# Kernel tuning notes

Hardware: AMD Instinct MI355X
Metric: run time of the kernel (lower is better)

Reference implementation:

```python
import jax, jax.numpy as jnp
import numpy as np

B, N_CLASS, N_CENTER, HIDDEN = 1024, 50, 8, 512
INIT_MU, BETA, EPS = 0.1, 0.5, 1e-8


def setup_inputs() -> dict:
    key = jax.random.key(0)
    k1, k2, k3, k4 = jax.random.split(key, 4)
    x = jax.random.normal(k1, (B, HIDDEN), dtype=jnp.float32)
    # class_mu ~ U(-init_mu, init_mu), matching torch.rand(...) * 2*init_mu - init_mu
    class_mu = jax.random.uniform(k2, (N_CLASS, N_CENTER, HIDDEN),
                                  minval=-INIT_MU, maxval=INIT_MU, dtype=jnp.float32)
    # binary dropout-style mask: (rand > beta).float()
    mask = (jax.random.uniform(k3, (N_CENTER, HIDDEN)) > BETA).astype(jnp.float32)
    # fixed random projection W ~ 0.1 * N(0,1)
    W = jax.random.normal(k4, (HIDDEN, HIDDEN), dtype=jnp.float32) * 0.1
    return {"x": x, "class_mu": class_mu, "mask": mask, "W": W}


def reference(x, class_mu, mask, W):
    # [B, n_center, hidden]: per-center masked copy of x, then shared projection W
    masked = x[:, None, :] * mask[None, :, :]
    mul = jnp.einsum('bch,hd->bcd', masked, W)
    # broadcast squared-distance against cluster centers: [B, n_class, n_center]
    diff = mul[:, None, :, :] - class_mu[None, :, :, :]  # [B, K, C, H]
    score = 1.0 / (1.0 + jnp.sum(diff * diff, axis=-1))  # Student-t style kernel
    # normalize over n_center (dim 2)
    distances = score / (jnp.sum(score, axis=2, keepdims=True) + EPS)
    # k_assign: second normalization over last dim (n_center)
    k_assign = distances / jnp.sum(distances, axis=-1, keepdims=True)
    return (mul, k_assign, distances)
```

## Files before the change

### kernel.cpp

```cpp
#include <hip/hip_runtime.h>

typedef short s16x8 __attribute__((ext_vector_type(8)));
typedef float f32x4 __attribute__((ext_vector_type(4)));

#define NB      1024
#define NCLASS  50
#define NCENTER 8
#define HID     512
#define KPAD    64
#define MROWS   8192

#define OFF_ABF    0u
#define OFF_WT     8388608u
#define OFF_MUBF   8912896u
#define OFF_MUNORM 9437184u
#define OFF_MULBF  9439232u
#define OFF_SCORE  17827840u

#define OUT_KA 4194304
#define OUT_D  4603904

__device__ __forceinline__ short f2bf(float f) {
    unsigned int u = __float_as_uint(f);
    unsigned int r = (u + 0x7FFFu + ((u >> 16) & 1u)) >> 16;
    return (short)(unsigned short)r;
}
__device__ __forceinline__ float bf2f(short h) {
    return __uint_as_float(((unsigned int)(unsigned short)h) << 16);
}

__global__ __launch_bounds__(256) void prep_kernel(
    const float* __restrict__ x, const float* __restrict__ class_mu,
    const float* __restrict__ mask, const float* __restrict__ W,
    short* __restrict__ Abf, short* __restrict__ WT,
    short* __restrict__ Mubf, float* __restrict__ Munorm)
{
    __shared__ float lds[64][65];
    const int blk = blockIdx.x, tid = threadIdx.x;

    if (blk < 256) {
        #pragma unroll
        for (int i = 0; i < 8; ++i) {
            int g = (blk * 256 + tid) + i * 65536;
            int e = g * 8;
            int r = e >> 9;
            int k = e & 511;
            int b = r >> 3, c = r & 7;
            const float4* xp = (const float4*)(x + b * HID + k);
            const float4* mp = (const float4*)(mask + c * HID + k);
            float4 x0 = xp[0], x1 = xp[1];
            float4 m0 = mp[0], m1 = mp[1];
            s16x8 o;
            o[0] = f2bf(x0.x * m0.x); o[1] = f2bf(x0.y * m0.y);
            o[2] = f2bf(x0.z * m0.z); o[3] = f2bf(x0.w * m0.w);
            o[4] = f2bf(x1.x * m1.x); o[5] = f2bf(x1.y * m1.y);
            o[6] = f2bf(x1.z * m1.z); o[7] = f2bf(x1.w * m1.w);
            *(s16x8*)(Abf + e) = o;
        }
    } else if (blk < 320) {
        int t = blk - 256;
        int th = t & 7, td = t >> 3;
        int col = tid & 63, rb = tid >> 6;
        #pragma unroll
        for (int it = 0; it < 16; ++it) {
            int row = it * 4 + rb;
            lds[row][col] = W[(th * 64 + row) * HID + td * 64 + col];
        }
        __syncthreads();
        #pragma unroll
        for (int it = 0; it < 16; ++it) {
            int row = it * 4 + rb;
            WT[(td * 64 + row) * HID + th * 64 + col] = f2bf(lds[col][row]);
        }
    } else {
        int w = (blk - 320) * 4 + (tid >> 6);
        int lane = tid & 63;
        int c = w >> 6, kk = w & 63;
        int h = lane * 8;
        float v[8];
        if (kk < NCLASS) {
            const float4* p = (const float4*)(class_mu + (kk * NCENTER + c) * HID + h);
            float4 a = p[0], bq = p[1];
            v[0] = a.x;  v[1] = a.y;  v[2] = a.z;  v[3] = a.w;
            v[4] = bq.x; v[5] = bq.y; v[6] = bq.z; v[7] = bq.w;
        } else {
            #pragma unroll
            for (int j = 0; j < 8; ++j) v[j] = 0.f;
        }
        s16x8 o; float sq = 0.f;
        #pragma unroll
        for (int j = 0; j < 8; ++j) { o[j] = f2bf(v[j]); sq += v[j] * v[j]; }
        *(s16x8*)(Mubf + (c * KPAD + kk) * HID + h) = o;
        sq += __shfl_xor(sq, 1);  sq += __shfl_xor(sq, 2);  sq += __shfl_xor(sq, 4);
        sq += __shfl_xor(sq, 8);  sq += __shfl_xor(sq, 16); sq += __shfl_xor(sq, 32);
        if (lane == 0) Munorm[c * KPAD + kk] = sq;
    }
}

__global__ __launch_bounds__(256) void gemm_mul(
    const short* __restrict__ Abf, const short* __restrict__ WT,
    float* __restrict__ mul_out, short* __restrict__ mulbf)
{
    __shared__ short As[128 * 32];
    __shared__ short Bs[128 * 32];
    const int tid = threadIdx.x;
    const int bm = blockIdx.x * 128;
    const int bn = blockIdx.y * 128;
    const int wave = tid >> 6, lane = tid & 63;
    const int wm = (wave & 1) * 64, wn = (wave >> 1) * 64;
    const int q = lane >> 4, l16 = lane & 15;

    f32x4 acc[4][4] = {};

    const int r0 = tid >> 2, c0 = (tid & 3) * 8;

    for (int it = 0; it < 16; ++it) {
        const int k0 = it * 32;
        *(s16x8*)(As + r0 * 32 + c0)        = *(const s16x8*)(Abf + (bm + r0) * HID + k0 + c0);
        *(s16x8*)(As + (r0 + 64) * 32 + c0) = *(const s16x8*)(Abf + (bm + r0 + 64) * HID + k0 + c0);
        *(s16x8*)(Bs + r0 * 32 + c0)        = *(const s16x8*)(WT + (bn + r0) * HID + k0 + c0);
        *(s16x8*)(Bs + (r0 + 64) * 32 + c0) = *(const s16x8*)(WT + (bn + r0 + 64) * HID + k0 + c0);
        __syncthreads();

        s16x8 af[4], bfr[4];
        #pragma unroll
        for (int mt = 0; mt < 4; ++mt)
            af[mt] = *(const s16x8*)(As + (wm + mt * 16 + l16) * 32 + q * 8);
        #pragma unroll
        for (int nt = 0; nt < 4; ++nt)
            bfr[nt] = *(const s16x8*)(Bs + (wn + nt * 16 + l16) * 32 + q * 8);
        #pragma unroll
        for (int mt = 0; mt < 4; ++mt)
            #pragma unroll
            for (int nt = 0; nt < 4; ++nt)
                acc[mt][nt] = __builtin_amdgcn_mfma_f32_16x16x32_bf16(af[mt], bfr[nt], acc[mt][nt], 0, 0, 0);
        __syncthreads();
    }

    #pragma unroll
    for (int mt = 0; mt < 4; ++mt) {
        #pragma unroll
        for (int nt = 0; nt < 4; ++nt) {
            #pragma unroll
            for (int reg = 0; reg < 4; ++reg) {
                int gr = bm + wm + mt * 16 + q * 4 + reg;
                int gc = bn + wn + nt * 16 + l16;
                float v = acc[mt][nt][reg];
                mul_out[gr * HID + gc] = v;
                mulbf[gr * HID + gc] = f2bf(v);
            }
        }
    }
}

__global__ __launch_bounds__(128) void score_kernel(
    const short* __restrict__ mulbf, const short* __restrict__ Mubf,
    const float* __restrict__ Munorm, float* __restrict__ score)
{
    const int tid = threadIdx.x;
    const int c = blockIdx.x & 7, bt = blockIdx.x >> 3;
    const int wave = tid >> 6, lane = tid & 63;
    const int q = lane >> 4, l16 = lane & 15;
    const int b0 = bt * 32 + wave * 16;

    f32x4 acc[4] = {};
    float nrm = 0.f;

    const short* arow = mulbf + ((b0 + l16) * NCENTER + c) * HID + q * 8;
    const short* brow = Mubf + (c * KPAD + l16) * HID + q * 8;

    for (int it = 0; it < 16; ++it) {
        const int k0 = it * 32;
        s16x8 av  = *(const s16x8*)(arow + k0);
        s16x8 bv0 = *(const s16x8*)(brow + k0);
        s16x8 bv1 = *(const s16x8*)(brow + 16 * HID + k0);
        s16x8 bv2 = *(const s16x8*)(brow + 32 * HID + k0);
        s16x8 bv3 = *(const s16x8*)(brow + 48 * HID + k0);
        #pragma unroll
        for (int j = 0; j < 8; ++j) { float f = bf2f(av[j]); nrm += f * f; }
        acc[0] = __builtin_amdgcn_mfma_f32_16x16x32_bf16(av, bv0, acc[0], 0, 0, 0);
        acc[1] = __builtin_amdgcn_mfma_f32_16x16x32_bf16(av, bv1, acc[1], 0, 0, 0);
        acc[2] = __builtin_amdgcn_mfma_f32_16x16x32_bf16(av, bv2, acc[2], 0, 0, 0);
        acc[3] = __builtin_amdgcn_mfma_f32_16x16x32_bf16(av, bv3, acc[3], 0, 0, 0);
    }

    nrm += __shfl_xor(nrm, 16);
    nrm += __shfl_xor(nrm, 32);
    float rowNorm[4];
    #pragma unroll
    for (int reg = 0; reg < 4; ++reg) rowNorm[reg] = __shfl(nrm, q * 4 + reg);

    #pragma unroll
    for (int nt = 0; nt < 4; ++nt) {
        float mn = Munorm[c * KPAD + nt * 16 + l16];
        #pragma unroll
        for (int reg = 0; reg < 4; ++reg) {
            float sq = rowNorm[reg] + mn - 2.f * acc[nt][reg];
            float sc = 1.f / (1.f + sq);
            int b = b0 + q * 4 + reg;
            int kcls = nt * 16 + l16;
            score[(b * KPAD + kcls) * NCENTER + c] = sc;
        }
    }
}

__global__ __launch_bounds__(256) void norm_kernel(
    const float* __restrict__ score, float* __restrict__ out)
{
    int t = blockIdx.x * 256 + threadIdx.x;
    if (t >= NB * NCLASS) return;
    int b = t / NCLASS, k = t % NCLASS;
    const float4* sp = (const float4*)(score + (b * KPAD + k) * NCENTER);
    float4 s0 = sp[0], s1 = sp[1];
    float S = s0.x + s0.y + s0.z + s0.w + s1.x + s1.y + s1.z + s1.w;
    float invd = 1.f / (S + 1e-8f);
    float invk = 1.f / S;
    float4 ka0, ka1, dd0, dd1;
    ka0.x = s0.x * invk; ka0.y = s0.y * invk; ka0.z = s0.z * invk; ka0.w = s0.w * invk;
    ka1.x = s1.x * invk; ka1.y = s1.y * invk; ka1.z = s1.z * invk; ka1.w = s1.w * invk;
    dd0.x = s0.x * invd; dd0.y = s0.y * invd; dd0.z = s0.z * invd; dd0.w = s0.w * invd;
    dd1.x = s1.x * invd; dd1.y = s1.y * invd; dd1.z = s1.z * invd; dd1.w = s1.w * invd;
    float* kap = out + OUT_KA + (b * NCLASS + k) * NCENTER;
    float* dp  = out + OUT_D  + (b * NCLASS + k) * NCENTER;
    ((float4*)kap)[0] = ka0; ((float4*)kap)[1] = ka1;
    ((float4*)dp)[0]  = dd0; ((float4*)dp)[1]  = dd1;
}

extern "C" void kernel_launch(void* const* d_in, const int* in_sizes, int n_in,
                              void* d_out, int out_size, void* d_ws, size_t ws_size,
                              hipStream_t stream) {
    const float* x        = (const float*)d_in[0];
    const float* class_mu = (const float*)d_in[1];
    const float* mask     = (const float*)d_in[2];
    const float* W        = (const float*)d_in[3];
    float* out = (float*)d_out;
    char* ws = (char*)d_ws;

    short* Abf    = (short*)(ws + OFF_ABF);
    short* WT     = (short*)(ws + OFF_WT);
    short* Mubf   = (short*)(ws + OFF_MUBF);
    float* Munorm = (float*)(ws + OFF_MUNORM);
    short* mulbf  = (short*)(ws + OFF_MULBF);
    float* score  = (float*)(ws + OFF_SCORE);

    prep_kernel<<<448, 256, 0, stream>>>(x, class_mu, mask, W, Abf, WT, Mubf, Munorm);
    gemm_mul<<<dim3(64, 4), 256, 0, stream>>>(Abf, WT, out, mulbf);
    score_kernel<<<256, 128, 0, stream>>>(mulbf, Mubf, Munorm, score);
    norm_kernel<<<200, 256, 0, stream>>>(score, out);
}
```

Before: 97.94 us.

## Fuse mask into GEMM load, compute row norms in epilogue, merge score and normalize

Prep now converts only x to bf16 plus a 16-bit mask, and the GEMM applies the mask with a bitwise AND while loading tiles. This avoids writing and reading the 8x-expanded masked input. The GEMM epilogue computes squared row norms of mul and accumulates them with atomics. The score and normalization kernels are merged into one, which handles all 8 centers per block and writes k_assign and distances directly, removing the intermediate score buffer. The cost is atomic contention, a row norm taken from fp32 accumulators rather than the bf16 values, and a score kernel with only 64 threads per block.

```diff
diff --git a/kernel.cpp b/kernel.cpp
--- a/kernel.cpp
+++ b/kernel.cpp
@@ -2,20 +2,21 @@
 
 typedef short s16x8 __attribute__((ext_vector_type(8)));
 typedef float f32x4 __attribute__((ext_vector_type(4)));
+typedef unsigned int u32x4 __attribute__((ext_vector_type(4)));
 
 #define NB      1024
 #define NCLASS  50
 #define NCENTER 8
 #define HID     512
 #define KPAD    64
-#define MROWS   8192
-
-#define OFF_ABF    0u
-#define OFF_WT     8388608u
-#define OFF_MUBF   8912896u
-#define OFF_MUNORM 9437184u
-#define OFF_MULBF  9439232u
-#define OFF_SCORE  17827840u
+
+#define OFF_XBF    0u
+#define OFF_MASK16 1048576u
+#define OFF_WT     1056768u
+#define OFF_MUBF   1581056u
+#define OFF_MUNT   2105344u
+#define OFF_MULBF  2107392u
+#define OFF_RNORM  10496000u
 
 #define OUT_KA 4194304
 #define OUT_D  4603904
@@ -25,40 +26,50 @@
     unsigned int r = (u + 0x7FFFu + ((u >> 16) & 1u)) >> 16;
     return (short)(unsigned short)r;
 }
-__device__ __forceinline__ float bf2f(short h) {
-    return __uint_as_float(((unsigned int)(unsigned short)h) << 16);
-}
 
 __global__ __launch_bounds__(256) void prep_kernel(
     const float* __restrict__ x, const float* __restrict__ class_mu,
     const float* __restrict__ mask, const float* __restrict__ W,
-    short* __restrict__ Abf, short* __restrict__ WT,
-    short* __restrict__ Mubf, float* __restrict__ Munorm)
+    short* __restrict__ xbf, short* __restrict__ mask16, short* __restrict__ WT,
+    short* __restrict__ Mubf, float* __restrict__ MunormT,
+    float* __restrict__ rowNorm)
 {
     __shared__ float lds[64][65];
     const int blk = blockIdx.x, tid = threadIdx.x;
 
-    if (blk < 256) {
+    if (blk < 32) {
         #pragma unroll
         for (int i = 0; i < 8; ++i) {
-            int g = (blk * 256 + tid) + i * 65536;
+            int g = (blk * 256 + tid) + i * 8192;
             int e = g * 8;
-            int r = e >> 9;
-            int k = e & 511;
-            int b = r >> 3, c = r & 7;
-            const float4* xp = (const float4*)(x + b * HID + k);
-            const float4* mp = (const float4*)(mask + c * HID + k);
-            float4 x0 = xp[0], x1 = xp[1];
-            float4 m0 = mp[0], m1 = mp[1];
+            const float4* xp = (const float4*)(x + e);
+            float4 a = xp[0], b = xp[1];
             s16x8 o;
-            o[0] = f2bf(x0.x * m0.x); o[1] = f2bf(x0.y * m0.y);
-            o[2] = f2bf(x0.z * m0.z); o[3] = f2bf(x0.w * m0.w);
-            o[4] = f2bf(x1.x * m1.x); o[5] = f2bf(x1.y * m1.y);
-            o[6] = f2bf(x1.z * m1.z); o[7] = f2bf(x1.w * m1.w);
-            *(s16x8*)(Abf + e) = o;
-        }
-    } else if (blk < 320) {
-        int t = blk - 256;
+            o[0] = f2bf(a.x); o[1] = f2bf(a.y); o[2] = f2bf(a.z); o[3] = f2bf(a.w);
+            o[4] = f2bf(b.x); o[5] = f2bf(b.y); o[6] = f2bf(b.z); o[7] = f2bf(b.w);
+            *(s16x8*)(xbf + e) = o;
+        }
+    } else if (blk == 32) {
+        int e = tid * 16;
+        const float4* mp = (const float4*)(mask + e);
+        float4 m0 = mp[0], m1 = mp[1], m2 = mp[2], m3 = mp[3];
+        s16x8 o0, o1;
+        o0[0] = (m0.x != 0.f) ? (short)0xFFFF : 0; o0[1] = (m0.y != 0.f) ? (short)0xFFFF : 0;
+        o0[2] = (m0.z != 0.f) ? (short)0xFFFF : 0; o0[3] = (m0.w != 0.f) ? (short)0xFFFF : 0;
+        o0[4] = (m1.x != 0.f) ? (short)0xFFFF : 0; o0[5] = (m1.y != 0.f) ? (short)0xFFFF : 0;
+        o0[6] = (m1.z != 0.f) ? (short)0xFFFF : 0; o0[7] = (m1.w != 0.f) ? (short)0xFFFF : 0;
+        o1[0] = (m2.x != 0.f) ? (short)0xFFFF : 0; o1[1] = (m2.y != 0.f) ? (short)0xFFFF : 0;
+        o1[2] = (m2.z != 0.f) ? (short)0xFFFF : 0; o1[3] = (m2.w != 0.f) ? (short)0xFFFF : 0;
+        o1[4] = (m3.x != 0.f) ? (short)0xFFFF : 0; o1[5] = (m3.y != 0.f) ? (short)0xFFFF : 0;
+        o1[6] = (m3.z != 0.f) ? (short)0xFFFF : 0; o1[7] = (m3.w != 0.f) ? (short)0xFFFF : 0;
+        *(s16x8*)(mask16 + e) = o0;
+        *(s16x8*)(mask16 + e + 8) = o1;
+        float4 z = {0.f, 0.f, 0.f, 0.f};
+        #pragma unroll
+        for (int j = 0; j < 8; ++j)
+            *(float4*)(rowNorm + (j * 256 + tid) * 4) = z;
+    } else if (blk < 97) {
+        int t = blk - 33;
         int th = t & 7, td = t >> 3;
         int col = tid & 63, rb = tid >> 6;
         #pragma unroll
@@ -73,7 +84,7 @@
             WT[(td * 64 + row) * HID + th * 64 + col] = f2bf(lds[col][row]);
         }
     } else {
-        int w = (blk - 320) * 4 + (tid >> 6);
+        int w = (blk - 97) * 4 + (tid >> 6);
         int lane = tid & 63;
         int c = w >> 6, kk = w & 63;
         int h = lane * 8;
@@ -93,13 +104,15 @@
         *(s16x8*)(Mubf + (c * KPAD + kk) * HID + h) = o;
         sq += __shfl_xor(sq, 1);  sq += __shfl_xor(sq, 2);  sq += __shfl_xor(sq, 4);
         sq += __shfl_xor(sq, 8);  sq += __shfl_xor(sq, 16); sq += __shfl_xor(sq, 32);
-        if (lane == 0) Munorm[c * KPAD + kk] = sq;
+        if (lane == 0) MunormT[kk * 8 + c] = sq;
     }
 }
 
 __global__ __launch_bounds__(256) void gemm_mul(
-    const short* __restrict__ Abf, const short* __restrict__ WT,
-    float* __restrict__ mul_out, short* __restrict__ mulbf)
+    const short* __restrict__ xbf, const short* __restrict__ mask16,
+    const short* __restrict__ WT,
+    float* __restrict__ mul_out, short* __restrict__ mulbf,
+    float* __restrict__ rowNorm)
 {
     __shared__ short As[128 * 32];
     __shared__ short Bs[128 * 32];
@@ -113,11 +126,17 @@
     f32x4 acc[4][4] = {};
 
     const int r0 = tid >> 2, c0 = (tid & 3) * 8;
+    const int bA0 = (bm >> 3) + (r0 >> 3);
+    const int bA1 = (bm >> 3) + ((r0 + 64) >> 3);
+    const int cA  = r0 & 7;
 
     for (int it = 0; it < 16; ++it) {
         const int k0 = it * 32;
-        *(s16x8*)(As + r0 * 32 + c0)        = *(const s16x8*)(Abf + (bm + r0) * HID + k0 + c0);
-        *(s16x8*)(As + (r0 + 64) * 32 + c0) = *(const s16x8*)(Abf + (bm + r0 + 64) * HID + k0 + c0);
+        u32x4 ma = *(const u32x4*)(mask16 + cA * HID + k0 + c0);
+        u32x4 x0 = *(const u32x4*)(xbf + bA0 * HID + k0 + c0);
+        u32x4 x1 = *(const u32x4*)(xbf + bA1 * HID + k0 + c0);
+        *(u32x4*)(As + r0 * 32 + c0)        = x0 & ma;
+        *(u32x4*)(As + (r0 + 64) * 32 + c0) = x1 & ma;
         *(s16x8*)(Bs + r0 * 32 + c0)        = *(const s16x8*)(WT + (bn + r0) * HID + k0 + c0);
         *(s16x8*)(Bs + (r0 + 64) * 32 + c0) = *(const s16x8*)(WT + (bn + r0 + 64) * HID + k0 + c0);
         __syncthreads();
@@ -151,79 +170,82 @@
             }
         }
     }
-}
-
-__global__ __launch_bounds__(128) void score_kernel(
+    #pragma unroll
+    for (int mt = 0; mt < 4; ++mt) {
+        #pragma unroll
+        for (int reg = 0; reg < 4; ++reg) {
+            float s = acc[mt][0][reg] * acc[mt][0][reg];
+            s += acc[mt][1][reg] * acc[mt][1][reg];
+            s += acc[mt][2][reg] * acc[mt][2][reg];
+            s += acc[mt][3][reg] * acc[mt][3][reg];
+            s += __shfl_xor(s, 1); s += __shfl_xor(s, 2);
+            s += __shfl_xor(s, 4); s += __shfl_xor(s, 8);
+            if (l16 == 0)
+                atomicAdd(&rowNorm[bm + wm + mt * 16 + q * 4 + reg], s);
+        }
+    }
+}
+
+__global__ __launch_bounds__(64) void scorenorm_kernel(
     const short* __restrict__ mulbf, const short* __restrict__ Mubf,
-    const float* __restrict__ Munorm, float* __restrict__ score)
+    const float* __restrict__ MunormT, const float* __restrict__ rowNorm,
+    float* __restrict__ out)
 {
-    const int tid = threadIdx.x;
-    const int c = blockIdx.x & 7, bt = blockIdx.x >> 3;
-    const int wave = tid >> 6, lane = tid & 63;
+    const int bt = blockIdx.x & 63, cg = blockIdx.x >> 6;
+    const int lane = threadIdx.x & 63;
     const int q = lane >> 4, l16 = lane & 15;
-    const int b0 = bt * 32 + wave * 16;
-
-    f32x4 acc[4] = {};
-    float nrm = 0.f;
-
-    const short* arow = mulbf + ((b0 + l16) * NCENTER + c) * HID + q * 8;
-    const short* brow = Mubf + (c * KPAD + l16) * HID + q * 8;
+    const int b0 = bt * 16, cls0 = cg * 16;
+
+    f32x4 acc[8] = {};
+    const short* arow = mulbf + (b0 + l16) * NCENTER * HID + q * 8;
+    const short* brow = Mubf + (cls0 + l16) * HID + q * 8;
 
     for (int it = 0; it < 16; ++it) {
         const int k0 = it * 32;
-        s16x8 av  = *(const s16x8*)(arow + k0);
-        s16x8 bv0 = *(const s16x8*)(brow + k0);
-        s16x8 bv1 = *(const s16x8*)(brow + 16 * HID + k0);
-        s16x8 bv2 = *(const s16x8*)(brow + 32 * HID + k0);
-        s16x8 bv3 = *(const s16x8*)(brow + 48 * HID + k0);
-        #pragma unroll
-        for (int j = 0; j < 8; ++j) { float f = bf2f(av[j]); nrm += f * f; }
-        acc[0] = __builtin_amdgcn_mfma_f32_16x16x32_bf16(av, bv0, acc[0], 0, 0, 0);
-        acc[1] = __builtin_amdgcn_mfma_f32_16x16x32_bf16(av, bv1, acc[1], 0, 0, 0);
-        acc[2] = __builtin_amdgcn_mfma_f32_16x16x32_bf16(av, bv2, acc[2], 0, 0, 0);
-        acc[3] = __builtin_amdgcn_mfma_f32_16x16x32_bf16(av, bv3, acc[3], 0, 0, 0);
-    }
-
-    nrm += __shfl_xor(nrm, 16);
-    nrm += __shfl_xor(nrm, 32);
-    float rowNorm[4];
+        s16x8 av[8], bv[8];
+        #pragma unroll
+        for (int c = 0; c < 8; ++c) av[c] = *(const s16x8*)(arow + c * HID + k0);
+        #pragma unroll
+        for (int c = 0; c < 8; ++c) bv[c] = *(const s16x8*)(brow + c * KPAD * HID + k0);
+        #pragma unroll
+        for (int c = 0; c < 8; ++c)
+            acc[c] = __builtin_amdgcn_mfma_f32_16x16x32_bf16(av[c], bv[c], acc[c], 0, 0, 0);
+    }
+
+    const int cls = cls0 + l16;
+    float4 mn0 = *(const float4*)(MunormT + cls * 8);
+    float4 mn1 = *(const float4*)(MunormT + cls * 8 + 4);
+    const float mn[8] = {mn0.x, mn0.y, mn0.z, mn0.w, mn1.x, mn1.y, mn1.z, mn1.w};
+
     #pragma unroll
-    for (int reg = 0; reg < 4; ++reg) rowNorm[reg] = __shfl(nrm, q * 4 + reg);
-
-    #pragma unroll
-    for (int nt = 0; nt < 4; ++nt) {
-        float mn = Munorm[c * KPAD + nt * 16 + l16];
-        #pragma unroll
-        for (int reg = 0; reg < 4; ++reg) {
-            float sq = rowNorm[reg] + mn - 2.f * acc[nt][reg];
-            float sc = 1.f / (1.f + sq);
-            int b = b0 + q * 4 + reg;
-            int kcls = nt * 16 + l16;
-            score[(b * KPAD + kcls) * NCENTER + c] = sc;
-        }
-    }
-}
-
-__global__ __launch_bounds__(256) void norm_kernel(
-    const float* __restrict__ score, float* __restrict__ out)
-{
-    int t = blockIdx.x * 256 + threadIdx.x;
-    if (t >= NB * NCLASS) return;
-    int b = t / NCLASS, k = t % NCLASS;
-    const float4* sp = (const float4*)(score + (b * KPAD + k) * NCENTER);
-    float4 s0 = sp[0], s1 = sp[1];
-    float S = s0.x + s0.y + s0.z + s0.w + s1.x + s1.y + s1.z + s1.w;
-    float invd = 1.f / (S + 1e-8f);
-    float invk = 1.f / S;
-    float4 ka0, ka1, dd0, dd1;
-    ka0.x = s0.x * invk; ka0.y = s0.y * invk; ka0.z = s0.z * invk; ka0.w = s0.w * invk;
-    ka1.x = s1.x * invk; ka1.y = s1.y * invk; ka1.z = s1.z * invk; ka1.w = s1.w * invk;
-    dd0.x = s0.x * invd; dd0.y = s0.y * invd; dd0.z = s0.z * invd; dd0.w = s0.w * invd;
-    dd1.x = s1.x * invd; dd1.y = s1.y * invd; dd1.z = s1.z * invd; dd1.w = s1.w * invd;
-    float* kap = out + OUT_KA + (b * NCLASS + k) * NCENTER;
-    float* dp  = out + OUT_D  + (b * NCLASS + k) * NCENTER;
-    ((float4*)kap)[0] = ka0; ((float4*)kap)[1] = ka1;
-    ((float4*)dp)[0]  = dd0; ((float4*)dp)[1]  = dd1;
+    for (int reg = 0; reg < 4; ++reg) {
+        const int b = b0 + q * 4 + reg;
+        float4 rn0 = *(const float4*)(rowNorm + b * 8);
+        float4 rn1 = *(const float4*)(rowNorm + b * 8 + 4);
+        const float rn[8] = {rn0.x, rn0.y, rn0.z, rn0.w, rn1.x, rn1.y, rn1.z, rn1.w};
+        float sc[8], S = 0.f;
+        #pragma unroll
+        for (int c = 0; c < 8; ++c) {
+            float sq = rn[c] + mn[c] - 2.f * acc[c][reg];
+            sc[c] = 1.f / (1.f + sq);
+            S += sc[c];
+        }
+        float invk = 1.f / S;
+        float invd = 1.f / (S + 1e-8f);
+        if (cls < NCLASS) {
+            float* kap = out + OUT_KA + (b * NCLASS + cls) * NCENTER;
+            float* dp  = out + OUT_D  + (b * NCLASS + cls) * NCENTER;
+            float4 o;
+            o.x = sc[0] * invk; o.y = sc[1] * invk; o.z = sc[2] * invk; o.w = sc[3] * invk;
+            ((float4*)kap)[0] = o;
+            o.x = sc[4] * invk; o.y = sc[5] * invk; o.z = sc[6] * invk; o.w = sc[7] * invk;
+            ((float4*)kap)[1] = o;
+            o.x = sc[0] * invd; o.y = sc[1] * invd; o.z = sc[2] * invd; o.w = sc[3] * invd;
+            ((float4*)dp)[0] = o;
+            o.x = sc[4] * invd; o.y = sc[5] * invd; o.z = sc[6] * invd; o.w = sc[7] * invd;
+            ((float4*)dp)[1] = o;
+        }
+    }
 }
 
 extern "C" void kernel_launch(void* const* d_in, const int* in_sizes, int n_in,
@@ -236,15 +258,16 @@
     float* out = (float*)d_out;
     char* ws = (char*)d_ws;
 
-    short* Abf    = (short*)(ws + OFF_ABF);
-    short* WT     = (short*)(ws + OFF_WT);
-    short* Mubf   = (short*)(ws + OFF_MUBF);
-    float* Munorm = (float*)(ws + OFF_MUNORM);
-    short* mulbf  = (short*)(ws + OFF_MULBF);
-    float* score  = (float*)(ws + OFF_SCORE);
-
-    prep_kernel<<<448, 256, 0, stream>>>(x, class_mu, mask, W, Abf, WT, Mubf, Munorm);
-    gemm_mul<<<dim3(64, 4), 256, 0, stream>>>(Abf, WT, out, mulbf);
-    score_kernel<<<256, 128, 0, stream>>>(mulbf, Mubf, Munorm, score);
-    norm_kernel<<<200, 256, 0, stream>>>(score, out);
-}
+    short* xbf     = (short*)(ws + OFF_XBF);
+    short* mask16  = (short*)(ws + OFF_MASK16);
+    short* WT      = (short*)(ws + OFF_WT);
+    short* Mubf    = (short*)(ws + OFF_MUBF);
+    float* MunormT = (float*)(ws + OFF_MUNT);
+    short* mulbf   = (short*)(ws + OFF_MULBF);
+    float* rowNorm = (float*)(ws + OFF_RNORM);
+
+    prep_kernel<<<225, 256, 0, stream>>>(x, class_mu, mask, W,
+                                         xbf, mask16, WT, Mubf, MunormT, rowNorm);
+    gemm_mul<<<dim3(64, 4), 256, 0, stream>>>(xbf, mask16, WT, out, mulbf, rowNorm);
+    scorenorm_kernel<<<256, 64, 0, stream>>>(mulbf, Mubf, MunormT, rowNorm, out);
+}
```

Result: slower. 101.6 us (+3.8%).
